# Performance work log

Hardware: AMD Instinct MI355X
Metric: run time of the kernel (lower is better)

Reference implementation:

```python
import jax, jax.numpy as jnp
import numpy as np
import math

N, DIN, H, D = 3072, 512, 16, 64
HD = H * D


def mish(x):
    return x * jnp.tanh(jax.nn.softplus(x))


def setup_inputs() -> dict:
    key = jax.random.key(0)
    ks = jax.random.split(key, 10)
    s_in = 1.0 / math.sqrt(DIN)
    s_hd = 1.0 / math.sqrt(HD)
    return {
        "q": jax.random.normal(ks[0], (N, DIN), jnp.float32),
        "k": jax.random.normal(ks[1], (N, DIN), jnp.float32),
        "v": jax.random.normal(ks[2], (N, DIN), jnp.float32),
        "bias": jax.random.normal(ks[3], (N, N), jnp.float32),
        "mask": jax.random.randint(ks[4], (N, N), 0, 2, jnp.int32),
        # q/k/v projections (xavier-like init, zero bias as in _reset_parameters)
        "Wq": jax.random.normal(ks[5], (HD, DIN), jnp.float32) * s_in,
        "bq": jnp.zeros((HD,), jnp.float32),
        "Wk": jax.random.normal(ks[6], (HD, DIN), jnp.float32) * s_in,
        "bk": jnp.zeros((HD,), jnp.float32),
        "Wv": jax.random.normal(ks[7], (HD, DIN), jnp.float32) * s_in,
        "bv": jnp.zeros((HD,), jnp.float32),
        # o_proj = Linear(HD,HD) -> Mish -> Linear(HD,DIN)
        "Wo1": jax.random.normal(ks[8], (HD, HD), jnp.float32) * s_hd,
        "bo1": jnp.zeros((HD,), jnp.float32),
        "Wo2": jax.random.normal(ks[9], (DIN, HD), jnp.float32) * s_hd,
        "bo2": jnp.zeros((DIN,), jnp.float32),
    }


def reference(q, k, v, bias, mask, Wq, bq, Wk, bk, Wv, bv, Wo1, bo1, Wo2, bo2):
    # forward(..., embed_bias=True, embed_value=True) path
    n = q.shape[0]
    # project and split heads: [N, DIN] -> [H, N, D]
    qh = (q @ Wq.T + bq).reshape(n, H, D).transpose(1, 0, 2)
    kh = (k @ Wk.T + bk).reshape(n, H, D).transpose(1, 0, 2)
    vh = (v @ Wv.T + bv).reshape(n, H, D).transpose(1, 0, 2)
    # scaled dot product with additive bias (broadcast over heads) + mask fill
    logits = jnp.einsum('hnd,hmd->hnm', qh, kh) / math.sqrt(D)
    logits = logits + bias[None, :, :]
    logits = jnp.where(mask[None, :, :] == 0, jnp.float32(-9e15), logits)
    attn = jax.nn.softmax(logits, axis=-1)           # [H, N, N]
    vals = jnp.einsum('hnm,hmd->hnd', attn, vh)      # [H, N, D]
    vals = vals.transpose(1, 0, 2).reshape(n, HD)    # [N, H*D]
    # o_proj MLP (dropout = 0)
    out = mish(vals @ Wo1.T + bo1) @ Wo2.T + bo2     # [N, DIN]
    return (out, bias)
```

## Files before the change

### kernel.cpp

```cpp
#include <hip/hip_runtime.h>
#include <hip/hip_bf16.h>

#define NT 3072
#define DIN_ 512
#define NH 16
#define DH 64
#define HDIM 1024

typedef unsigned short u16;
typedef unsigned int u32;
typedef short short8 __attribute__((ext_vector_type(8)));
typedef float f32x4 __attribute__((ext_vector_type(4)));
typedef __bf16 bf16x8 __attribute__((ext_vector_type(8)));

__device__ __forceinline__ u16 f2bf(float f){
  union { float f; unsigned u; } v; v.f = f;
  unsigned r = v.u + 0x7fffu + ((v.u >> 16) & 1u);
  return (u16)(r >> 16);
}
__device__ __forceinline__ float bf2f(u16 b){
  union { unsigned u; float f; } v; v.u = ((unsigned)b) << 16;
  return v.f;
}

__global__ __launch_bounds__(256) void prep_k(
    const float* __restrict__ bias, const int* __restrict__ mask,
    u16* __restrict__ bm, float* __restrict__ bias_out)
{
  int i = blockIdx.x * 256 + threadIdx.x;
  f32x4 b = ((const f32x4*)bias)[i];
  int4 m = ((const int4*)mask)[i];
  ((f32x4*)bias_out)[i] = b;
  const int mm[4] = {m.x, m.y, m.z, m.w};
  union { u16 s[4]; unsigned long long ll; } pk;
  #pragma unroll
  for (int j = 0; j < 4; ++j)
    pk.s[j] = mm[j] ? f2bf(b[j]) : f2bf(-1e30f);
  ((unsigned long long*)bm)[i] = pk.ll;
}

template<int A_BF16, int EPI>
__device__ __forceinline__ void gemm_body(
    const void* __restrict__ Aptr, const float* __restrict__ W,
    const float* __restrict__ bvec, void* __restrict__ Cptr,
    int Nc, int K, float scale, int bm0, int bn0,
    u16* As, u16* Bs)
{
  const int tid = threadIdx.x;
  const int lane = tid & 63;
  const int wid = tid >> 6;
  const int wr = wid >> 1, wc = wid & 1;
  const int g = lane >> 4, lr = lane & 15;

  f32x4 acc[4][4] = {};

  for (int k0 = 0; k0 < K; k0 += 32) {
    __syncthreads();
    if (A_BF16) {
      const u16* A = (const u16*)Aptr;
      #pragma unroll
      for (int it = 0; it < 2; ++it) {
        int e = it*2048 + tid*8;
        int r = e >> 5, kk = e & 31;
        *(short8*)&As[r*40 + kk] = *(const short8*)&A[(size_t)(bm0+r)*K + k0 + kk];
      }
    } else {
      const float* A = (const float*)Aptr;
      #pragma unroll
      for (int it = 0; it < 4; ++it) {
        int e = it*1024 + tid*4;
        int r = e >> 5, kk = e & 31;
        f32x4 v = *(const f32x4*)&A[(size_t)(bm0+r)*K + k0 + kk];
        union { u16 s[4]; unsigned long long ll; } pk;
        #pragma unroll
        for (int jj = 0; jj < 4; ++jj) pk.s[jj] = f2bf(v[jj]);
        *(unsigned long long*)&As[r*40 + kk] = pk.ll;
      }
    }
    {
      #pragma unroll
      for (int it = 0; it < 4; ++it) {
        int e = it*1024 + tid*4;
        int r = e >> 5, kk = e & 31;
        f32x4 v = *(const f32x4*)&W[(size_t)(bn0+r)*K + k0 + kk];
        union { u16 s[4]; unsigned long long ll; } pk;
        #pragma unroll
        for (int jj = 0; jj < 4; ++jj) pk.s[jj] = f2bf(v[jj]);
        *(unsigned long long*)&Bs[r*40 + kk] = pk.ll;
      }
    }
    __syncthreads();
    bf16x8 af[4], bfr[4];
    #pragma unroll
    for (int m = 0; m < 4; ++m)
      af[m] = *(const bf16x8*)&As[(wr*64 + m*16 + lr)*40 + g*8];
    #pragma unroll
    for (int n = 0; n < 4; ++n)
      bfr[n] = *(const bf16x8*)&Bs[(wc*64 + n*16 + lr)*40 + g*8];
    #pragma unroll
    for (int m = 0; m < 4; ++m)
      #pragma unroll
      for (int n = 0; n < 4; ++n)
        acc[m][n] = __builtin_amdgcn_mfma_f32_16x16x32_bf16(af[m], bfr[n], acc[m][n], 0, 0, 0);
  }

  #pragma unroll
  for (int m = 0; m < 4; ++m) {
    const int row0 = bm0 + wr*64 + m*16 + g*4;
    #pragma unroll
    for (int n = 0; n < 4; ++n) {
      const int col = bn0 + wc*64 + n*16 + lr;
      const float bb = bvec[col];
      #pragma unroll
      for (int j = 0; j < 4; ++j) {
        float x = acc[m][n][j] + bb;
        if (EPI == 0) x *= scale;
        if (EPI == 1) {
          float sp = (x > 15.f) ? x : log1pf(__expf(x));
          x = x * tanhf(sp);
        }
        if (EPI == 2)
          ((float*)Cptr)[(size_t)(row0+j)*Nc + col] = x;
        else
          ((u16*)Cptr)[(size_t)(row0+j)*Nc + col] = f2bf(x);
      }
    }
  }
}

template<int A_BF16, int EPI>
__global__ __launch_bounds__(256) void gemm_k(
    const void* __restrict__ Aptr, const float* __restrict__ W,
    const float* __restrict__ bvec, void* __restrict__ Cptr,
    int Nc, int K, float scale)
{
  __shared__ __align__(16) u16 As[128*40];
  __shared__ __align__(16) u16 Bs[128*40];
  gemm_body<A_BF16, EPI>(Aptr, W, bvec, Cptr, Nc, K, scale,
                         blockIdx.x*128, blockIdx.y*128, As, Bs);
}

__global__ __launch_bounds__(256) void qkv_k(
    const float* __restrict__ q, const float* __restrict__ k,
    const float* __restrict__ v,
    const float* __restrict__ Wq, const float* __restrict__ bq,
    const float* __restrict__ Wk, const float* __restrict__ bk,
    const float* __restrict__ Wv, const float* __restrict__ bv,
    u16* __restrict__ qh, u16* __restrict__ kh, u16* __restrict__ vh)
{
  __shared__ __align__(16) u16 As[128*40];
  __shared__ __align__(16) u16 Bs[128*40];
  const int sel = blockIdx.y >> 3;
  const float* A    = sel == 0 ? q  : (sel == 1 ? k  : v);
  const float* W    = sel == 0 ? Wq : (sel == 1 ? Wk : Wv);
  const float* bvec = sel == 0 ? bq : (sel == 1 ? bk : bv);
  u16* C            = sel == 0 ? qh : (sel == 1 ? kh : vh);
  const float scale = sel == 0 ? 0.125f : 1.0f;
  gemm_body<0, 0>(A, W, bvec, C, HDIM, DIN_, scale,
                  blockIdx.x*128, (blockIdx.y & 7)*128, As, Bs);
}

__global__ __launch_bounds__(256) void attn_k(
    const u16* __restrict__ qh, const u16* __restrict__ kh,
    const u16* __restrict__ vh, const u16* __restrict__ bm,
    u16* __restrict__ vals)
{
  __shared__ __align__(16) u16 Qs[64*72];
  __shared__ __align__(16) u16 Ks[64*72];
  __shared__ __align__(16) u16 Vts[64*72];
  __shared__ __align__(16) u16 Bms[64*72];
  __shared__ __align__(16) u16 Ps[4][16*72];

  const int tid = threadIdx.x;
  const int lane = tid & 63;
  const int w = tid >> 6;
  const int g = lane >> 4, lr = lane & 15;
  const int i0 = blockIdx.x * 64;
  const int hoff = blockIdx.y * DH;

  #pragma unroll
  for (int it = 0; it < 2; ++it) {
    int c = it*256 + tid;
    int r = c >> 3, co = (c & 7) * 8;
    *(short8*)&Qs[r*72 + co] = *(const short8*)&qh[(size_t)(i0 + r)*HDIM + hoff + co];
  }
  __syncthreads();
  bf16x8 qf[2];
  #pragma unroll
  for (int kc = 0; kc < 2; ++kc)
    qf[kc] = *(const bf16x8*)&Qs[(w*16 + lr)*72 + kc*32 + g*8];

  f32x4 Oa[4] = {};
  float mrow[4], lsum[4];
  #pragma unroll
  for (int r = 0; r < 4; ++r) { mrow[r] = -1e30f; lsum[r] = 0.f; }

  for (int j = 0; j < NT/64; ++j) {
    __syncthreads();
    const int c0 = j * 64;
    #pragma unroll
    for (int it = 0; it < 2; ++it) {
      int c = it*256 + tid;
      int r = c >> 3, co = (c & 7) * 8;
      *(short8*)&Ks[r*72 + co] = *(const short8*)&kh[(size_t)(c0 + r)*HDIM + hoff + co];
    }
    #pragma unroll
    for (int it = 0; it < 2; ++it) {
      int c = it*256 + tid;
      int r = c >> 3, co = (c & 7) * 8;
      *(short8*)&Bms[r*72 + co] = *(const short8*)&bm[(size_t)(i0 + r)*NT + c0 + co];
    }
    #pragma unroll
    for (int it = 0; it < 2; ++it) {
      int c = it*256 + tid;
      int vr = c >> 3, dco = (c & 7) * 8;
      short8 v = *(const short8*)&vh[(size_t)(c0 + vr)*HDIM + hoff + dco];
      #pragma unroll
      for (int jj = 0; jj < 8; ++jj) {
        int d = dco + jj;
        int byte = d*144 + vr*2;
        byte ^= ((d >> 3) & 7) << 4;
        *(u16*)((char*)Vts + byte) = (u16)v[jj];
      }
    }
    __syncthreads();

    f32x4 Sa[4] = {};
    #pragma unroll
    for (int kc = 0; kc < 2; ++kc) {
      #pragma unroll
      for (int n = 0; n < 4; ++n) {
        bf16x8 kb = *(const bf16x8*)&Ks[(n*16 + lr)*72 + kc*32 + g*8];
        Sa[n] = __builtin_amdgcn_mfma_f32_16x16x32_bf16(qf[kc], kb, Sa[n], 0, 0, 0);
      }
    }
    float P[4][4];
    float alpha[4];
    #pragma unroll
    for (int jr = 0; jr < 4; ++jr) {
      const int r = g*4 + jr;
      float s0[4];
      float tmax = -1e30f;
      #pragma unroll
      for (int n = 0; n < 4; ++n) {
        float bb = bf2f(Bms[(w*16 + r)*72 + n*16 + lr]);
        float s = Sa[n][jr] + bb;
        s0[n] = s;
        tmax = fmaxf(tmax, s);
      }
      #pragma unroll
      for (int msk = 1; msk < 16; msk <<= 1)
        tmax = fmaxf(tmax, __shfl_xor(tmax, msk, 64));
      float mnew = fmaxf(mrow[jr], tmax);
      alpha[jr] = __expf(mrow[jr] - mnew);
      float psum = 0.f;
      #pragma unroll
      for (int n = 0; n < 4; ++n) {
        float p = __expf(s0[n] - mnew);
        P[n][jr] = p;
        psum += p;
      }
      #pragma unroll
      for (int msk = 1; msk < 16; msk <<= 1)
        psum += __shfl_xor(psum, msk, 64);
      lsum[jr] = lsum[jr]*alpha[jr] + psum;
      mrow[jr] = mnew;
    }
    #pragma unroll
    for (int n = 0; n < 4; ++n)
      #pragma unroll
      for (int jr = 0; jr < 4; ++jr)
        Oa[n][jr] *= alpha[jr];
    #pragma unroll
    for (int n = 0; n < 4; ++n)
      #pragma unroll
      for (int jr = 0; jr < 4; ++jr)
        Ps[w][(g*4 + jr)*72 + n*16 + lr] = f2bf(P[n][jr]);
    __asm__ volatile("s_waitcnt lgkmcnt(0)" ::: "memory");
    __builtin_amdgcn_sched_barrier(0);
    #pragma unroll
    for (int kc = 0; kc < 2; ++kc) {
      bf16x8 pa = *(const bf16x8*)&Ps[w][lr*72 + kc*32 + g*8];
      #pragma unroll
      for (int n = 0; n < 4; ++n) {
        int d = n*16 + lr;
        int byte = d*144 + (kc*32 + g*8)*2;
        byte ^= ((d >> 3) & 7) << 4;
        bf16x8 vb = *(const bf16x8*)((const char*)Vts + byte);
        Oa[n] = __builtin_amdgcn_mfma_f32_16x16x32_bf16(pa, vb, Oa[n], 0, 0, 0);
      }
    }
  }

  #pragma unroll
  for (int n = 0; n < 4; ++n) {
    #pragma unroll
    for (int jr = 0; jr < 4; ++jr) {
      float o = Oa[n][jr] / lsum[jr];
      int row = i0 + w*16 + g*4 + jr;
      vals[(size_t)row*HDIM + hoff + n*16 + lr] = f2bf(o);
    }
  }
}

extern "C" void kernel_launch(void* const* d_in, const int* in_sizes, int n_in,
                              void* d_out, int out_size, void* d_ws, size_t ws_size,
                              hipStream_t stream) {
  const float* q    = (const float*)d_in[0];
  const float* k    = (const float*)d_in[1];
  const float* v    = (const float*)d_in[2];
  const float* bias = (const float*)d_in[3];
  const int*   mask = (const int*)d_in[4];
  const float* Wq   = (const float*)d_in[5];
  const float* bq   = (const float*)d_in[6];
  const float* Wk   = (const float*)d_in[7];
  const float* bk   = (const float*)d_in[8];
  const float* Wv   = (const float*)d_in[9];
  const float* bv   = (const float*)d_in[10];
  const float* Wo1  = (const float*)d_in[11];
  const float* bo1  = (const float*)d_in[12];
  const float* Wo2  = (const float*)d_in[13];
  const float* bo2  = (const float*)d_in[14];

  float* out = (float*)d_out;
  float* bias_out = out + (size_t)NT * DIN_;

  char* ws = (char*)d_ws;
  u16* bm   = (u16*)ws; ws += (size_t)NT*NT*2;
  u16* qh   = (u16*)ws; ws += (size_t)NT*HDIM*2;
  u16* kh   = (u16*)ws; ws += (size_t)NT*HDIM*2;
  u16* vh   = (u16*)ws; ws += (size_t)NT*HDIM*2;
  u16* vals = (u16*)ws; ws += (size_t)NT*HDIM*2;
  u16* t1   = qh;

  prep_k<<<dim3(NT*NT/4/256), 256, 0, stream>>>(bias, mask, bm, bias_out);

  qkv_k<<<dim3(NT/128, 24), 256, 0, stream>>>(q, k, v, Wq, bq, Wk, bk, Wv, bv,
                                              qh, kh, vh);

  attn_k<<<dim3(NT/64, NH), 256, 0, stream>>>(qh, kh, vh, bm, vals);

  gemm_k<1,1><<<dim3(NT/128, HDIM/128), 256, 0, stream>>>(vals, Wo1, bo1, t1, HDIM, HDIM, 1.0f);
  gemm_k<1,2><<<dim3(NT/128, DIN_/128), 256, 0, stream>>>(t1, Wo2, bo2, out, DIN_, HDIM, 1.0f);
}
```

Before: 486.1 us.

## Pre-convert weights to bf16 and transpose QK^T so softmax rows live per lane

Adds a kernel that converts all projection weights to bf16 once, so the GEMMs load bf16 weight tiles directly instead of converting fp32 on every tile. In the attention kernel the S=QK^T MFMA operands are swapped so each lane holds a full query row across columns. The bias/mask tile is loaded straight from global into the accumulator init, which removes the Bms shared buffer, and the row max and sum reductions drop from four shuffle steps to two. Alpha and the final normaliser are redistributed with shuffles to match the O accumulator layout. The cost is one extra small launch plus extra workspace, and uncoalesced per-lane bias loads from global memory.

```diff
diff --git a/kernel.cpp b/kernel.cpp
--- a/kernel.cpp
+++ b/kernel.cpp
@@ -39,9 +39,32 @@
   ((unsigned long long*)bm)[i] = pk.ll;
 }
 
+__global__ __launch_bounds__(256) void cvtw_k(
+    const float* __restrict__ Wq, const float* __restrict__ Wk,
+    const float* __restrict__ Wv, const float* __restrict__ Wo1,
+    const float* __restrict__ Wo2,
+    u16* __restrict__ wqb, u16* __restrict__ wkb, u16* __restrict__ wvb,
+    u16* __restrict__ wo1b, u16* __restrict__ wo2b)
+{
+  const float* src; u16* dst; int n4;
+  switch (blockIdx.y) {
+    case 0: src = Wq;  dst = wqb;  n4 = HDIM*DIN_/4; break;
+    case 1: src = Wk;  dst = wkb;  n4 = HDIM*DIN_/4; break;
+    case 2: src = Wv;  dst = wvb;  n4 = HDIM*DIN_/4; break;
+    case 3: src = Wo1; dst = wo1b; n4 = HDIM*HDIM/4; break;
+    default: src = Wo2; dst = wo2b; n4 = DIN_*HDIM/4; break;
+  }
+  int i = blockIdx.x * 256 + threadIdx.x;
+  if (i >= n4) return;
+  f32x4 v = ((const f32x4*)src)[i];
+  ushort4 o;
+  o.x = f2bf(v[0]); o.y = f2bf(v[1]); o.z = f2bf(v[2]); o.w = f2bf(v[3]);
+  ((ushort4*)dst)[i] = o;
+}
+
 template<int A_BF16, int EPI>
 __device__ __forceinline__ void gemm_body(
-    const void* __restrict__ Aptr, const float* __restrict__ W,
+    const void* __restrict__ Aptr, const u16* __restrict__ W,
     const float* __restrict__ bvec, void* __restrict__ Cptr,
     int Nc, int K, float scale, int bm0, int bn0,
     u16* As, u16* Bs)
@@ -79,14 +102,10 @@
     }
     {
       #pragma unroll
-      for (int it = 0; it < 4; ++it) {
-        int e = it*1024 + tid*4;
+      for (int it = 0; it < 2; ++it) {
+        int e = it*2048 + tid*8;
         int r = e >> 5, kk = e & 31;
-        f32x4 v = *(const f32x4*)&W[(size_t)(bn0+r)*K + k0 + kk];
-        union { u16 s[4]; unsigned long long ll; } pk;
-        #pragma unroll
-        for (int jj = 0; jj < 4; ++jj) pk.s[jj] = f2bf(v[jj]);
-        *(unsigned long long*)&Bs[r*40 + kk] = pk.ll;
+        *(short8*)&Bs[r*40 + kk] = *(const short8*)&W[(size_t)(bn0+r)*K + k0 + kk];
       }
     }
     __syncthreads();
@@ -130,7 +149,7 @@
 
 template<int A_BF16, int EPI>
 __global__ __launch_bounds__(256) void gemm_k(
-    const void* __restrict__ Aptr, const float* __restrict__ W,
+    const void* __restrict__ Aptr, const u16* __restrict__ W,
     const float* __restrict__ bvec, void* __restrict__ Cptr,
     int Nc, int K, float scale)
 {
@@ -143,18 +162,18 @@
 __global__ __launch_bounds__(256) void qkv_k(
     const float* __restrict__ q, const float* __restrict__ k,
     const float* __restrict__ v,
-    const float* __restrict__ Wq, const float* __restrict__ bq,
-    const float* __restrict__ Wk, const float* __restrict__ bk,
-    const float* __restrict__ Wv, const float* __restrict__ bv,
+    const u16* __restrict__ wqb, const float* __restrict__ bq,
+    const u16* __restrict__ wkb, const float* __restrict__ bk,
+    const u16* __restrict__ wvb, const float* __restrict__ bv,
     u16* __restrict__ qh, u16* __restrict__ kh, u16* __restrict__ vh)
 {
   __shared__ __align__(16) u16 As[128*40];
   __shared__ __align__(16) u16 Bs[128*40];
   const int sel = blockIdx.y >> 3;
-  const float* A    = sel == 0 ? q  : (sel == 1 ? k  : v);
-  const float* W    = sel == 0 ? Wq : (sel == 1 ? Wk : Wv);
-  const float* bvec = sel == 0 ? bq : (sel == 1 ? bk : bv);
-  u16* C            = sel == 0 ? qh : (sel == 1 ? kh : vh);
+  const float* A    = sel == 0 ? q   : (sel == 1 ? k   : v);
+  const u16* W      = sel == 0 ? wqb : (sel == 1 ? wkb : wvb);
+  const float* bvec = sel == 0 ? bq  : (sel == 1 ? bk  : bv);
+  u16* C            = sel == 0 ? qh  : (sel == 1 ? kh  : vh);
   const float scale = sel == 0 ? 0.125f : 1.0f;
   gemm_body<0, 0>(A, W, bvec, C, HDIM, DIN_, scale,
                   blockIdx.x*128, (blockIdx.y & 7)*128, As, Bs);
@@ -168,7 +187,6 @@
   __shared__ __align__(16) u16 Qs[64*72];
   __shared__ __align__(16) u16 Ks[64*72];
   __shared__ __align__(16) u16 Vts[64*72];
-  __shared__ __align__(16) u16 Bms[64*72];
   __shared__ __align__(16) u16 Ps[4][16*72];
 
   const int tid = threadIdx.x;
@@ -191,13 +209,12 @@
     qf[kc] = *(const bf16x8*)&Qs[(w*16 + lr)*72 + kc*32 + g*8];
 
   f32x4 Oa[4] = {};
-  float mrow[4], lsum[4];
-  #pragma unroll
-  for (int r = 0; r < 4; ++r) { mrow[r] = -1e30f; lsum[r] = 0.f; }
+  float mr = -1e30f, ls = 0.f;
+  const size_t bmrow = (size_t)(i0 + w*16 + lr) * NT;
 
   for (int j = 0; j < NT/64; ++j) {
+    const int c0 = j * 64;
     __syncthreads();
-    const int c0 = j * 64;
     #pragma unroll
     for (int it = 0; it < 2; ++it) {
       int c = it*256 + tid;
@@ -207,77 +224,77 @@
     #pragma unroll
     for (int it = 0; it < 2; ++it) {
       int c = it*256 + tid;
-      int r = c >> 3, co = (c & 7) * 8;
-      *(short8*)&Bms[r*72 + co] = *(const short8*)&bm[(size_t)(i0 + r)*NT + c0 + co];
-    }
-    #pragma unroll
-    for (int it = 0; it < 2; ++it) {
-      int c = it*256 + tid;
       int vr = c >> 3, dco = (c & 7) * 8;
-      short8 v = *(const short8*)&vh[(size_t)(c0 + vr)*HDIM + hoff + dco];
+      short8 vv = *(const short8*)&vh[(size_t)(c0 + vr)*HDIM + hoff + dco];
       #pragma unroll
       for (int jj = 0; jj < 8; ++jj) {
         int d = dco + jj;
         int byte = d*144 + vr*2;
         byte ^= ((d >> 3) & 7) << 4;
-        *(u16*)((char*)Vts + byte) = (u16)v[jj];
+        *(u16*)((char*)Vts + byte) = (u16)vv[jj];
       }
     }
     __syncthreads();
 
-    f32x4 Sa[4] = {};
-    #pragma unroll
-    for (int kc = 0; kc < 2; ++kc) {
+    f32x4 Sa[4];
+    #pragma unroll
+    for (int n = 0; n < 4; ++n) {
+      ushort4 bb = *(const ushort4*)&bm[bmrow + c0 + n*16 + g*4];
+      Sa[n][0] = bf2f(bb.x); Sa[n][1] = bf2f(bb.y);
+      Sa[n][2] = bf2f(bb.z); Sa[n][3] = bf2f(bb.w);
+    }
+    #pragma unroll
+    for (int kc = 0; kc < 2; ++kc)
       #pragma unroll
       for (int n = 0; n < 4; ++n) {
         bf16x8 kb = *(const bf16x8*)&Ks[(n*16 + lr)*72 + kc*32 + g*8];
-        Sa[n] = __builtin_amdgcn_mfma_f32_16x16x32_bf16(qf[kc], kb, Sa[n], 0, 0, 0);
-      }
-    }
-    float P[4][4];
-    float alpha[4];
-    #pragma unroll
-    for (int jr = 0; jr < 4; ++jr) {
-      const int r = g*4 + jr;
-      float s0[4];
-      float tmax = -1e30f;
-      #pragma unroll
-      for (int n = 0; n < 4; ++n) {
-        float bb = bf2f(Bms[(w*16 + r)*72 + n*16 + lr]);
-        float s = Sa[n][jr] + bb;
-        s0[n] = s;
-        tmax = fmaxf(tmax, s);
-      }
-      #pragma unroll
-      for (int msk = 1; msk < 16; msk <<= 1)
-        tmax = fmaxf(tmax, __shfl_xor(tmax, msk, 64));
-      float mnew = fmaxf(mrow[jr], tmax);
-      alpha[jr] = __expf(mrow[jr] - mnew);
-      float psum = 0.f;
-      #pragma unroll
-      for (int n = 0; n < 4; ++n) {
-        float p = __expf(s0[n] - mnew);
-        P[n][jr] = p;
-        psum += p;
-      }
-      #pragma unroll
-      for (int msk = 1; msk < 16; msk <<= 1)
-        psum += __shfl_xor(psum, msk, 64);
-      lsum[jr] = lsum[jr]*alpha[jr] + psum;
-      mrow[jr] = mnew;
-    }
+        Sa[n] = __builtin_amdgcn_mfma_f32_16x16x32_bf16(kb, qf[kc], Sa[n], 0, 0, 0);
+      }
+
+    float tmax = -1e30f;
     #pragma unroll
     for (int n = 0; n < 4; ++n)
       #pragma unroll
       for (int jr = 0; jr < 4; ++jr)
-        Oa[n][jr] *= alpha[jr];
+        tmax = fmaxf(tmax, Sa[n][jr]);
+    tmax = fmaxf(tmax, __shfl_xor(tmax, 16, 64));
+    tmax = fmaxf(tmax, __shfl_xor(tmax, 32, 64));
+    float mnew = fmaxf(mr, tmax);
+    float alpha_me = __expf(mr - mnew);
+    mr = mnew;
+    float ps = 0.f;
     #pragma unroll
     for (int n = 0; n < 4; ++n)
       #pragma unroll
+      for (int jr = 0; jr < 4; ++jr) {
+        float p = __expf(Sa[n][jr] - mnew);
+        Sa[n][jr] = p;
+        ps += p;
+      }
+    ps += __shfl_xor(ps, 16, 64);
+    ps += __shfl_xor(ps, 32, 64);
+    ls = ls * alpha_me + ps;
+
+    float av[4];
+    #pragma unroll
+    for (int jr = 0; jr < 4; ++jr)
+      av[jr] = __shfl(alpha_me, g*4 + jr, 16);
+    #pragma unroll
+    for (int n = 0; n < 4; ++n)
+      #pragma unroll
       for (int jr = 0; jr < 4; ++jr)
-        Ps[w][(g*4 + jr)*72 + n*16 + lr] = f2bf(P[n][jr]);
+        Oa[n][jr] *= av[jr];
+
+    #pragma unroll
+    for (int n = 0; n < 4; ++n) {
+      ushort4 pk;
+      pk.x = f2bf(Sa[n][0]); pk.y = f2bf(Sa[n][1]);
+      pk.z = f2bf(Sa[n][2]); pk.w = f2bf(Sa[n][3]);
+      *(ushort4*)&Ps[w][lr*72 + n*16 + g*4] = pk;
+    }
     __asm__ volatile("s_waitcnt lgkmcnt(0)" ::: "memory");
     __builtin_amdgcn_sched_barrier(0);
+
     #pragma unroll
     for (int kc = 0; kc < 2; ++kc) {
       bf16x8 pa = *(const bf16x8*)&Ps[w][lr*72 + kc*32 + g*8];
@@ -292,11 +309,15 @@
     }
   }
 
+  float lv[4];
+  #pragma unroll
+  for (int jr = 0; jr < 4; ++jr)
+    lv[jr] = 1.f / __shfl(ls, g*4 + jr, 16);
   #pragma unroll
   for (int n = 0; n < 4; ++n) {
     #pragma unroll
     for (int jr = 0; jr < 4; ++jr) {
-      float o = Oa[n][jr] / lsum[jr];
+      float o = Oa[n][jr] * lv[jr];
       int row = i0 + w*16 + g*4 + jr;
       vals[(size_t)row*HDIM + hoff + n*16 + lr] = f2bf(o);
     }
@@ -326,20 +347,27 @@
   float* bias_out = out + (size_t)NT * DIN_;
 
   char* ws = (char*)d_ws;
-  u16* bm   = (u16*)ws; ws += (size_t)NT*NT*2;
-  u16* qh   = (u16*)ws; ws += (size_t)NT*HDIM*2;
-  u16* kh   = (u16*)ws; ws += (size_t)NT*HDIM*2;
-  u16* vh   = (u16*)ws; ws += (size_t)NT*HDIM*2;
-  u16* vals = (u16*)ws; ws += (size_t)NT*HDIM*2;
-  u16* t1   = qh;
-
+  u16* bm    = (u16*)ws; ws += (size_t)NT*NT*2;
+  u16* qh    = (u16*)ws; ws += (size_t)NT*HDIM*2;
+  u16* kh    = (u16*)ws; ws += (size_t)NT*HDIM*2;
+  u16* vh    = (u16*)ws; ws += (size_t)NT*HDIM*2;
+  u16* vals  = (u16*)ws; ws += (size_t)NT*HDIM*2;
+  u16* wqb   = (u16*)ws; ws += (size_t)HDIM*DIN_*2;
+  u16* wkb   = (u16*)ws; ws += (size_t)HDIM*DIN_*2;
+  u16* wvb   = (u16*)ws; ws += (size_t)HDIM*DIN_*2;
+  u16* wo1b  = (u16*)ws; ws += (size_t)HDIM*HDIM*2;
+  u16* wo2b  = (u16*)ws; ws += (size_t)DIN_*HDIM*2;
+  u16* t1    = qh;
+
+  cvtw_k<<<dim3(1024, 5), 256, 0, stream>>>(Wq, Wk, Wv, Wo1, Wo2,
+                                            wqb, wkb, wvb, wo1b, wo2b);
   prep_k<<<dim3(NT*NT/4/256), 256, 0, stream>>>(bias, mask, bm, bias_out);
 
-  qkv_k<<<dim3(NT/128, 24), 256, 0, stream>>>(q, k, v, Wq, bq, Wk, bk, Wv, bv,
+  qkv_k<<<dim3(NT/128, 24), 256, 0, stream>>>(q, k, v, wqb, bq, wkb, bk, wvb, bv,
                                               qh, kh, vh);
 
   attn_k<<<dim3(NT/64, NH), 256, 0, stream>>>(qh, kh, vh, bm, vals);
 
-  gemm_k<1,1><<<dim3(NT/128, HDIM/128), 256, 0, stream>>>(vals, Wo1, bo1, t1, HDIM, HDIM, 1.0f);
-  gemm_k<1,2><<<dim3(NT/128, DIN_/128), 256, 0, stream>>>(t1, Wo2, bo2, out, DIN_, HDIM, 1.0f);
-}
+  gemm_k<1,1><<<dim3(NT/128, HDIM/128), 256, 0, stream>>>(vals, wo1b, bo1, t1, HDIM, HDIM, 1.0f);
+  gemm_k<1,2><<<dim3(NT/128, DIN_/128), 256, 0, stream>>>(t1, wo2b, bo2, out, DIN_, HDIM, 1.0f);
+}
```

New measurement: 418.1 us. -14.0%, faster.
